# Optimization experiments

Hardware: AMD Instinct MI355X
Metric: run time of the kernel (lower is better)

Reference implementation:

```python
import jax, jax.numpy as jnp
import numpy as np

B, T, C = 2, 2048, 2048
N_HEAD, N_KV = 16, 4
HD = C // N_HEAD          # 128
ROPE_THETA = 10000.0


def setup_inputs() -> dict:
    key = jax.random.key(0)
    ks = jax.random.split(key, 6)
    std = 0.02
    x = jax.random.normal(ks[0], (B, T, C), dtype=jnp.float32)
    Wq = jax.random.normal(ks[1], (C, C), dtype=jnp.float32) * std
    Wk = jax.random.normal(ks[2], (C, N_KV * HD), dtype=jnp.float32) * std
    Wv = jax.random.normal(ks[3], (C, N_KV * HD), dtype=jnp.float32) * std
    Wo = jax.random.normal(ks[4], (C, C), dtype=jnp.float32) * std
    # real RoPE frequencies: freqs_cis = exp(i * t * theta^{-2j/hd})
    inv_freq = 1.0 / (ROPE_THETA ** (jnp.arange(0, HD, 2, dtype=jnp.float32) / HD))
    ang = jnp.arange(T, dtype=jnp.float32)[:, None] * inv_freq[None, :]  # [T, HD//2]
    return {"x": x, "Wq": Wq, "Wk": Wk, "Wv": Wv, "Wo": Wo,
            "freqs_cos": jnp.cos(ang), "freqs_sin": jnp.sin(ang)}


def _rope(t, cos, sin):
    # t: [B, H, T, HD]; cos/sin: [T, HD//2] -> complex rotate even/odd pairs
    tr = t.reshape(*t.shape[:-1], HD // 2, 2)
    re, im = tr[..., 0], tr[..., 1]
    c = cos[None, None, :, :]
    s = sin[None, None, :, :]
    out = jnp.stack([re * c - im * s, re * s + im * c], axis=-1)
    return out.reshape(t.shape)


def reference(x, Wq, Wk, Wv, Wo, freqs_cos, freqs_sin):
    Bm, Tm, Cm = x.shape
    q = (x @ Wq).reshape(Bm, Tm, N_HEAD, HD).transpose(0, 2, 1, 3)  # [B,H,T,HD]
    k = (x @ Wk).reshape(Bm, Tm, N_KV, HD).transpose(0, 2, 1, 3)    # [B,Hkv,T,HD]
    v = (x @ Wv).reshape(Bm, Tm, N_KV, HD).transpose(0, 2, 1, 3)
    q = _rope(q, freqs_cos, freqs_sin)
    k = _rope(k, freqs_cos, freqs_sin)
    rep = N_HEAD // N_KV
    k = jnp.repeat(k, rep, axis=1)  # GQA repeat_kv -> [B,H,T,HD]
    v = jnp.repeat(v, rep, axis=1)
    scale = 1.0 / jnp.sqrt(jnp.asarray(HD, dtype=x.dtype))
    att = jnp.einsum("bhqd,bhkd->bhqk", q, k) * scale
    causal = jnp.tril(jnp.ones((Tm, Tm), dtype=bool))
    att = jnp.where(causal[None, None], att, jnp.asarray(-jnp.inf, att.dtype))
    att = jax.nn.softmax(att, axis=-1)
    y = jnp.einsum("bhqk,bhkd->bhqd", att, v)
    y = y.transpose(0, 2, 1, 3).reshape(Bm, Tm, Cm)
    return y @ Wo
```

## Files before the change

### kernel.cpp

```cpp
#include <hip/hip_runtime.h>

#define B_ 2
#define T_ 2048
#define C_ 2048
#define NH_ 16
#define NKV_ 4
#define HD_ 128
#define REP_ (NH_ / NKV_)
#define LDQKV 3072

typedef unsigned short u16;
typedef __bf16 bf16x8v __attribute__((ext_vector_type(8)));
typedef float f32x4v __attribute__((ext_vector_type(4)));

__device__ __forceinline__ u16 f2bf(float f) {
    unsigned int u;
    __builtin_memcpy(&u, &f, 4);
    u += 0x7FFFu + ((u >> 16) & 1u);
    return (u16)(u >> 16);
}
__device__ __forceinline__ unsigned int pk2(float a, float b) {
    unsigned int ua, ub;
    __builtin_memcpy(&ua, &a, 4);
    __builtin_memcpy(&ub, &b, 4);
    ua += 0x8000u; ub += 0x8000u;
    return (ua >> 16) | (ub & 0xFFFF0000u);
}
__device__ __forceinline__ bf16x8v load8(const u16* p) {
    return *reinterpret_cast<const bf16x8v*>(p);
}
__device__ __forceinline__ void gl16(const u16* g, u16* l) {
    __builtin_amdgcn_global_load_lds(
        (const __attribute__((address_space(1))) void*)(g),
        (__attribute__((address_space(3))) void*)(l), 16, 0, 0);
}

__global__ void cvt_f32_bf16(const float* __restrict__ in, u16* __restrict__ out, int n4) {
    int i = blockIdx.x * blockDim.x + threadIdx.x;
    if (i >= n4) return;
    float4 v = reinterpret_cast<const float4*>(in)[i];
    ushort4 o;
    o.x = f2bf(v.x); o.y = f2bf(v.y); o.z = f2bf(v.z); o.w = f2bf(v.w);
    reinterpret_cast<ushort4*>(out)[i] = o;
}

__global__ void xpose_f32_bf16(const float* __restrict__ in, u16* __restrict__ out,
                               int R, int Cc) {
    __shared__ u16 tile[32][33];
    int bx = blockIdx.x * 32, by = blockIdx.y * 32;
    int tx = threadIdx.x, ty = threadIdx.y;
    for (int i = 0; i < 32; i += 8)
        tile[ty + i][tx] = f2bf(in[(size_t)(by + ty + i) * Cc + bx + tx]);
    __syncthreads();
    for (int i = 0; i < 32; i += 8)
        out[(size_t)(bx + ty + i) * R + by + tx] = tile[tx][ty + i];
}

__global__ __launch_bounds__(256) void gemm_qkv(const u16* __restrict__ A,
                                                const u16* __restrict__ BT,
                                                u16* __restrict__ Cq,
                                                u16* __restrict__ vtb,
                                                const float* __restrict__ cb,
                                                const float* __restrict__ sb,
                                                int M, int N, int K) {
    __shared__ __align__(16) u16 As[128 * 64];
    __shared__ __align__(16) u16 Bs[128 * 64];
    int tid = threadIdx.x;
    int lane = tid & 63, wave = tid >> 6;
    int wm = wave & 1, wn = wave >> 1;
    int m15 = lane & 15, quad = lane >> 4;
    int m0 = blockIdx.y * 128, n0 = blockIdx.x * 128;

    int r_ = tid >> 3, c_ = tid & 7;
    int gch = c_ ^ (r_ & 7);
    const u16* gA = A + (size_t)(m0 + r_) * K + gch * 8;
    const u16* gB = BT + (size_t)(n0 + r_) * K + gch * 8;
    u16* lA = As + tid * 8;
    u16* lB = Bs + tid * 8;

    int sw8 = m15 & 7;
    const u16* a0 = As + (wm * 64 + m15) * 64;
    const u16* b0 = Bs + (wn * 64 + m15) * 64;

    f32x4v acc[4][4] = {};
    for (int k0 = 0; k0 < K; k0 += 64) {
        __syncthreads();
        for (int j = 0; j < 4; j++) {
            gl16(gA + (size_t)(32 * j) * K, lA + j * 2048);
            gl16(gB + (size_t)(32 * j) * K, lB + j * 2048);
        }
        gA += 64; gB += 64;
        __syncthreads();
        for (int kc = 0; kc < 2; kc++) {
            int co = ((kc * 4 + quad) ^ sw8) * 8;
            bf16x8v af[4], bfv[4];
            for (int t = 0; t < 4; t++) {
                af[t] = load8(a0 + t * 1024 + co);
                bfv[t] = load8(b0 + t * 1024 + co);
            }
            for (int mt = 0; mt < 4; mt++)
                for (int nt = 0; nt < 4; nt++)
                    acc[mt][nt] = __builtin_amdgcn_mfma_f32_16x16x32_bf16(
                        af[mt], bfv[nt], acc[mt][nt], 0, 0, 0);
        }
    }

    if (n0 >= 2560) {
        for (int mt = 0; mt < 4; mt++)
            for (int nt = 0; nt < 4; nt++) {
                int hd = n0 + wn * 64 + nt * 16 + m15 - 2560;
                int mbase = m0 + wm * 64 + mt * 16 + quad * 4;
                int bb = mbase >> 11, tok = mbase & 2047;
                int g = (tok & 31) >> 2;
                int off = (tok & ~31) + ((g & 3) * 8 + (g >> 2) * 4);
                ushort4 pk;
                pk.x = f2bf(acc[mt][nt][0]);
                pk.y = f2bf(acc[mt][nt][1]);
                pk.z = f2bf(acc[mt][nt][2]);
                pk.w = f2bf(acc[mt][nt][3]);
                *reinterpret_cast<ushort4*>(vtb + ((size_t)bb * 512 + hd) * T_ + off) = pk;
            }
    } else {
        for (int mt = 0; mt < 4; mt++)
            for (int nt = 0; nt < 4; nt++) {
                int c = n0 + wn * 64 + nt * 16 + m15;
                int i = (c & 127) >> 1;
                float sgn = (c & 1) ? 1.f : -1.f;
                for (int r = 0; r < 4; r++) {
                    int mrow = m0 + wm * 64 + mt * 16 + quad * 4 + r;
                    int tok = mrow & 2047;
                    float cv = cb[tok * 64 + i];
                    float sv = sb[tok * 64 + i];
                    float v = acc[mt][nt][r];
                    float pval = __shfl_xor(v, 1, 64);
                    float outv = fmaf(v, cv, pval * sv * sgn);
                    Cq[(size_t)mrow * N + c] = f2bf(outv);
                }
            }
    }
}

__global__ __launch_bounds__(256) void gemm_out(const u16* __restrict__ A,
                                                const u16* __restrict__ BT,
                                                float* __restrict__ C,
                                                int M, int N, int K) {
    __shared__ __align__(16) u16 As[128 * 64];
    __shared__ __align__(16) u16 Bs[128 * 64];
    int tid = threadIdx.x;
    int lane = tid & 63, wave = tid >> 6;
    int wm = wave & 1, wn = wave >> 1;
    int m15 = lane & 15, quad = lane >> 4;
    int m0 = blockIdx.y * 128, n0 = blockIdx.x * 128;

    int r_ = tid >> 3, c_ = tid & 7;
    int gch = c_ ^ (r_ & 7);
    const u16* gA = A + (size_t)(m0 + r_) * K + gch * 8;
    const u16* gB = BT + (size_t)(n0 + r_) * K + gch * 8;
    u16* lA = As + tid * 8;
    u16* lB = Bs + tid * 8;

    int sw8 = m15 & 7;
    const u16* a0 = As + (wm * 64 + m15) * 64;
    const u16* b0 = Bs + (wn * 64 + m15) * 64;

    f32x4v acc[4][4] = {};
    for (int k0 = 0; k0 < K; k0 += 64) {
        __syncthreads();
        for (int j = 0; j < 4; j++) {
            gl16(gA + (size_t)(32 * j) * K, lA + j * 2048);
            gl16(gB + (size_t)(32 * j) * K, lB + j * 2048);
        }
        gA += 64; gB += 64;
        __syncthreads();
        for (int kc = 0; kc < 2; kc++) {
            int co = ((kc * 4 + quad) ^ sw8) * 8;
            bf16x8v af[4], bfv[4];
            for (int t = 0; t < 4; t++) {
                af[t] = load8(a0 + t * 1024 + co);
                bfv[t] = load8(b0 + t * 1024 + co);
            }
            for (int mt = 0; mt < 4; mt++)
                for (int nt = 0; nt < 4; nt++)
                    acc[mt][nt] = __builtin_amdgcn_mfma_f32_16x16x32_bf16(
                        af[mt], bfv[nt], acc[mt][nt], 0, 0, 0);
        }
    }

    for (int mt = 0; mt < 4; mt++)
        for (int nt = 0; nt < 4; nt++) {
            int c = n0 + wn * 64 + nt * 16 + m15;
            for (int r = 0; r < 4; r++) {
                int mrow = m0 + wm * 64 + mt * 16 + quad * 4 + r;
                C[(size_t)mrow * N + c] = acc[mt][nt][r];
            }
        }
}

__device__ __forceinline__ void stage_k128(const u16* kB, u16* Kl, int kt, int tid) {
    int keyc = tid >> 4, ch = tid & 15;
    const u16* g = kB + (size_t)(kt + keyc) * LDQKV + (ch ^ keyc) * 8;
    u16* l = Kl + tid * 8;
    for (int j = 0; j < 8; j++) {
        gl16(g, l);
        g += (size_t)16 * LDQKV;
        l += 2048;
    }
}
__device__ __forceinline__ void stage_v128(const u16* vB, u16* Vl, int kt, int tid) {
    int hdc = tid >> 4, ch = tid & 15;
    const u16* g = vB + (size_t)hdc * T_ + kt + (ch ^ hdc) * 8;
    u16* l = Vl + tid * 8;
    for (int j = 0; j < 8; j++) {
        gl16(g, l);
        g += (size_t)16 * T_;
        l += 2048;
    }
}

__global__ __launch_bounds__(256) void flash_k(const u16* __restrict__ qkv,
                                               const u16* __restrict__ vtb,
                                               u16* __restrict__ yb) {
    __shared__ __align__(16) u16 Kl[128 * 128];
    __shared__ __align__(16) u16 Vl[128 * 128];
    int h = blockIdx.y, b = blockIdx.z;
    int kv = h / REP_;
    int tid = threadIdx.x;
    int lane = tid & 63, wave = tid >> 6;
    int m15 = lane & 15, quad = lane >> 4;
    const u16* kB = qkv + (size_t)b * T_ * LDQKV + 2048 + kv * HD_;
    const u16* vB = vtb + ((size_t)(b * NKV_ + kv)) * HD_ * T_;
    const float scale2 = 0.1275173723f;
    const float M0b = 8.0f;
    const float NEG = -3.0e38f;

    for (int p = 0; p < 2; p++) {
        int qt = (p == 0) ? (int)blockIdx.x : (31 - (int)blockIdx.x);
        int qt0 = qt * 64;
        int qrow = qt0 + wave * 16;
        int q_i = qrow + m15;
        const u16* qp = qkv + (size_t)(b * T_ + q_i) * LDQKV + h * HD_ + quad * 8;
        bf16x8v qf[4];
        for (int kc = 0; kc < 4; kc++) qf[kc] = load8(qp + kc * 32);
        f32x4v o[8] = {};
        f32x4v lacc = {};

        int iters = qt0 / 128 + 1;
        for (int it = 0; it < iters; it++) {
            int kt = it * 128;
            __syncthreads();
            stage_k128(kB, Kl, kt, tid);
            stage_v128(vB, Vl, kt, tid);
            __syncthreads();
            f32x4v s4[8];
            for (int nt = 0; nt < 8; nt++) s4[nt] = (f32x4v){0.f, 0.f, 0.f, 0.f};
            for (int nt = 0; nt < 8; nt++) {
                const u16* kls = Kl + (nt * 16 + m15) * 128;
                for (int kc = 0; kc < 4; kc++)
                    s4[nt] = __builtin_amdgcn_mfma_f32_16x16x32_bf16(
                        load8(kls + (((kc * 4 + quad) ^ m15) * 8)), qf[kc], s4[nt], 0, 0, 0);
            }
            if (kt + 128 > qt0) {
                for (int nt = 0; nt < 8; nt++) {
                    int key = kt + nt * 16 + quad * 4;
                    for (int r = 0; r < 4; r++)
                        if (key + r > q_i) s4[nt][r] = NEG;
                }
            }
            for (int nt = 0; nt < 8; nt++) {
                for (int r = 0; r < 4; r++)
                    s4[nt][r] = exp2f(fmaf(s4[nt][r], scale2, -M0b));
                lacc += s4[nt];
            }
            for (int c = 0; c < 4; c++) {
                unsigned int w[4];
                w[0] = pk2(s4[2 * c][0], s4[2 * c][1]);
                w[1] = pk2(s4[2 * c][2], s4[2 * c][3]);
                w[2] = pk2(s4[2 * c + 1][0], s4[2 * c + 1][1]);
                w[3] = pk2(s4[2 * c + 1][2], s4[2 * c + 1][3]);
                bf16x8v pf;
                __builtin_memcpy(&pf, w, 16);
                for (int dt = 0; dt < 8; dt++) {
                    const u16* vls = Vl + (dt * 16 + m15) * 128;
                    o[dt] = __builtin_amdgcn_mfma_f32_16x16x32_bf16(
                        load8(vls + (((c * 4 + quad) ^ m15) * 8)), pf, o[dt], 0, 0, 0);
                }
            }
        }
        float l = lacc[0] + lacc[1] + lacc[2] + lacc[3];
        l += __shfl_xor(l, 16, 64);
        l += __shfl_xor(l, 32, 64);
        float inv = 1.f / l;
        u16* yp = yb + (size_t)(b * T_ + q_i) * C_ + h * HD_ + quad * 4;
        for (int dt = 0; dt < 8; dt++) {
            ushort4 pk;
            pk.x = f2bf(o[dt][0] * inv);
            pk.y = f2bf(o[dt][1] * inv);
            pk.z = f2bf(o[dt][2] * inv);
            pk.w = f2bf(o[dt][3] * inv);
            *reinterpret_cast<ushort4*>(yp + dt * 16) = pk;
        }
    }
}

extern "C" void kernel_launch(void* const* d_in, const int* in_sizes, int n_in,
                              void* d_out, int out_size, void* d_ws, size_t ws_size,
                              hipStream_t stream) {
    const float* x  = (const float*)d_in[0];
    const float* Wq = (const float*)d_in[1];
    const float* Wk = (const float*)d_in[2];
    const float* Wv = (const float*)d_in[3];
    const float* Wo = (const float*)d_in[4];
    const float* fc = (const float*)d_in[5];
    const float* fs = (const float*)d_in[6];
    float* out = (float*)d_out;

    char* ws = (char*)d_ws;
    u16* WqkvT = (u16*)(ws);
    u16* WoT   = (u16*)(ws + 12582912);
    u16* xb    = (u16*)(ws + 20971520);
    u16* qkvb  = (u16*)(ws + 37748736);
    u16* vtb   = (u16*)(ws + 62914560);
    u16* yb    = (u16*)(ws + 67108864);

    const int M = B_ * T_;

    int n4 = (M * C_) / 4;
    cvt_f32_bf16<<<n4 / 256, 256, 0, stream>>>(x, xb, n4);

    dim3 tb(32, 8);
    xpose_f32_bf16<<<dim3(C_ / 32, C_ / 32), tb, 0, stream>>>(Wq, WqkvT, C_, C_);
    xpose_f32_bf16<<<dim3((NKV_ * HD_) / 32, C_ / 32), tb, 0, stream>>>(Wk, WqkvT + 2048 * 2048, C_, NKV_ * HD_);
    xpose_f32_bf16<<<dim3((NKV_ * HD_) / 32, C_ / 32), tb, 0, stream>>>(Wv, WqkvT + 2560 * 2048, C_, NKV_ * HD_);
    xpose_f32_bf16<<<dim3(C_ / 32, C_ / 32), tb, 0, stream>>>(Wo, WoT, C_, C_);

    gemm_qkv<<<dim3(LDQKV / 128, M / 128), 256, 0, stream>>>(xb, WqkvT, qkvb, vtb, fc, fs, M, LDQKV, C_);

    flash_k<<<dim3(T_ / 128, NH_, B_), 256, 0, stream>>>(qkvb, vtb, yb);

    gemm_out<<<dim3(C_ / 128, M / 128), 256, 0, stream>>>(yb, WoT, out, M, C_, C_);
}
```

Measured before the change: 310.1 us.

## Use 256x256 double-buffered GEMM tiles with swizzled block order

Both projection GEMMs move from 128x128 tiles with 4 waves to 256x256 tiles with 8 waves. Each wave now computes a 128x64 sub-tile. Loads use a two-stage LDS double buffer with explicit vmcnt waits, so global fetches overlap MFMA work. A 1D grid with an XCD-aware block swizzle improves L2 locality, and setprio raises MFMA priority. In exchange, LDS use rises to 128KB per block and register pressure grows. Grid counts shrink: 192 blocks for QKV and 128 for the output GEMM, which may underfill the 256 CUs.

```diff
diff --git a/kernel.cpp b/kernel.cpp
--- a/kernel.cpp
+++ b/kernel.cpp
@@ -56,60 +56,94 @@
         out[(size_t)(bx + ty + i) * R + by + tx] = tile[tx][ty + i];
 }
 
-__global__ __launch_bounds__(256) void gemm_qkv(const u16* __restrict__ A,
-                                                const u16* __restrict__ BT,
-                                                u16* __restrict__ Cq,
-                                                u16* __restrict__ vtb,
-                                                const float* __restrict__ cb,
-                                                const float* __restrict__ sb,
-                                                int M, int N, int K) {
-    __shared__ __align__(16) u16 As[128 * 64];
-    __shared__ __align__(16) u16 Bs[128 * 64];
+__device__ __forceinline__ void stage_ab(const u16* gA, const u16* gB,
+                                         u16* As, u16* Bs, int tid, int K) {
+    u16* lA = As + tid * 8;
+    u16* lB = Bs + tid * 8;
+#pragma unroll
+    for (int j = 0; j < 4; j++) gl16(gA + (size_t)(64 * j) * K, lA + j * 4096);
+#pragma unroll
+    for (int j = 0; j < 4; j++) gl16(gB + (size_t)(64 * j) * K, lB + j * 4096);
+}
+
+__global__ __launch_bounds__(512, 2) void gemm_qkv(const u16* __restrict__ A,
+                                                   const u16* __restrict__ BT,
+                                                   u16* __restrict__ Cq,
+                                                   u16* __restrict__ vtb,
+                                                   const float* __restrict__ cb,
+                                                   const float* __restrict__ sb,
+                                                   int M, int N, int K) {
+    __shared__ __align__(16) u16 As[2][256 * 64];
+    __shared__ __align__(16) u16 Bs[2][256 * 64];
     int tid = threadIdx.x;
     int lane = tid & 63, wave = tid >> 6;
-    int wm = wave & 1, wn = wave >> 1;
+    int wm = wave >> 2, wn = wave & 3;
     int m15 = lane & 15, quad = lane >> 4;
-    int m0 = blockIdx.y * 128, n0 = blockIdx.x * 128;
+
+    int nbx = N >> 8;
+    int nwg = gridDim.x;
+    int bid = blockIdx.x;
+    int cpx = nwg >> 3;
+    int swz = (bid & 7) * cpx + (bid >> 3);
+    int bx = swz % nbx, by = swz / nbx;
+    int m0 = by * 256, n0 = bx * 256;
 
     int r_ = tid >> 3, c_ = tid & 7;
-    int gch = c_ ^ (r_ & 7);
-    const u16* gA = A + (size_t)(m0 + r_) * K + gch * 8;
-    const u16* gB = BT + (size_t)(n0 + r_) * K + gch * 8;
-    u16* lA = As + tid * 8;
-    u16* lB = Bs + tid * 8;
+    const u16* gA = A + (size_t)(m0 + r_) * K + (c_ ^ (r_ & 7)) * 8;
+    const u16* gB = BT + (size_t)(n0 + r_) * K + (c_ ^ (r_ & 7)) * 8;
 
     int sw8 = m15 & 7;
-    const u16* a0 = As + (wm * 64 + m15) * 64;
-    const u16* b0 = Bs + (wn * 64 + m15) * 64;
-
-    f32x4v acc[4][4] = {};
-    for (int k0 = 0; k0 < K; k0 += 64) {
-        __syncthreads();
-        for (int j = 0; j < 4; j++) {
-            gl16(gA + (size_t)(32 * j) * K, lA + j * 2048);
-            gl16(gB + (size_t)(32 * j) * K, lB + j * 2048);
-        }
-        gA += 64; gB += 64;
-        __syncthreads();
+    const u16* a0b = &As[0][0] + (wm * 128 + m15) * 64;
+    const u16* b0b = &Bs[0][0] + (wn * 64 + m15) * 64;
+
+    f32x4v acc[8][4] = {};
+
+    stage_ab(gA, gB, As[0], Bs[0], tid, K);
+    __builtin_amdgcn_sched_barrier(0);
+    stage_ab(gA + 64, gB + 64, As[1], Bs[1], tid, K);
+    asm volatile("s_waitcnt vmcnt(8)" ::: "memory");
+    __builtin_amdgcn_sched_barrier(0);
+    __builtin_amdgcn_s_barrier();
+
+    int NT = K >> 6;
+    for (int t = 0; t < NT; t++) {
+        const u16* a0 = a0b + (t & 1) * (256 * 64);
+        const u16* b0 = b0b + (t & 1) * (256 * 64);
+#pragma unroll
         for (int kc = 0; kc < 2; kc++) {
             int co = ((kc * 4 + quad) ^ sw8) * 8;
-            bf16x8v af[4], bfv[4];
-            for (int t = 0; t < 4; t++) {
-                af[t] = load8(a0 + t * 1024 + co);
-                bfv[t] = load8(b0 + t * 1024 + co);
-            }
-            for (int mt = 0; mt < 4; mt++)
+            bf16x8v bfv[4], af[8];
+#pragma unroll
+            for (int nt = 0; nt < 4; nt++) bfv[nt] = load8(b0 + nt * 1024 + co);
+#pragma unroll
+            for (int mt = 0; mt < 8; mt++) af[mt] = load8(a0 + mt * 1024 + co);
+            __builtin_amdgcn_s_setprio(1);
+#pragma unroll
+            for (int mt = 0; mt < 8; mt++)
+#pragma unroll
                 for (int nt = 0; nt < 4; nt++)
                     acc[mt][nt] = __builtin_amdgcn_mfma_f32_16x16x32_bf16(
                         af[mt], bfv[nt], acc[mt][nt], 0, 0, 0);
-        }
+            __builtin_amdgcn_s_setprio(0);
+        }
+        __builtin_amdgcn_s_barrier();
+        if (t + 2 < NT) {
+            stage_ab(gA + (t + 2) * 64, gB + (t + 2) * 64, As[t & 1], Bs[t & 1], tid, K);
+            asm volatile("s_waitcnt vmcnt(8)" ::: "memory");
+        } else {
+            asm volatile("s_waitcnt vmcnt(0)" ::: "memory");
+        }
+        __builtin_amdgcn_sched_barrier(0);
+        __builtin_amdgcn_s_barrier();
     }
 
     if (n0 >= 2560) {
-        for (int mt = 0; mt < 4; mt++)
+#pragma unroll
+        for (int mt = 0; mt < 8; mt++)
+#pragma unroll
             for (int nt = 0; nt < 4; nt++) {
                 int hd = n0 + wn * 64 + nt * 16 + m15 - 2560;
-                int mbase = m0 + wm * 64 + mt * 16 + quad * 4;
+                int mbase = m0 + wm * 128 + mt * 16 + quad * 4;
                 int bb = mbase >> 11, tok = mbase & 2047;
                 int g = (tok & 31) >> 2;
                 int off = (tok & ~31) + ((g & 3) * 8 + (g >> 2) * 4);
@@ -121,13 +155,16 @@
                 *reinterpret_cast<ushort4*>(vtb + ((size_t)bb * 512 + hd) * T_ + off) = pk;
             }
     } else {
-        for (int mt = 0; mt < 4; mt++)
+#pragma unroll
+        for (int mt = 0; mt < 8; mt++)
+#pragma unroll
             for (int nt = 0; nt < 4; nt++) {
                 int c = n0 + wn * 64 + nt * 16 + m15;
                 int i = (c & 127) >> 1;
                 float sgn = (c & 1) ? 1.f : -1.f;
+#pragma unroll
                 for (int r = 0; r < 4; r++) {
-                    int mrow = m0 + wm * 64 + mt * 16 + quad * 4 + r;
+                    int mrow = m0 + wm * 128 + mt * 16 + quad * 4 + r;
                     int tok = mrow & 2047;
                     float cv = cb[tok * 64 + i];
                     float sv = sb[tok * 64 + i];
@@ -140,57 +177,82 @@
     }
 }
 
-__global__ __launch_bounds__(256) void gemm_out(const u16* __restrict__ A,
-                                                const u16* __restrict__ BT,
-                                                float* __restrict__ C,
-                                                int M, int N, int K) {
-    __shared__ __align__(16) u16 As[128 * 64];
-    __shared__ __align__(16) u16 Bs[128 * 64];
+__global__ __launch_bounds__(512, 2) void gemm_out(const u16* __restrict__ A,
+                                                   const u16* __restrict__ BT,
+                                                   float* __restrict__ C,
+                                                   int M, int N, int K) {
+    __shared__ __align__(16) u16 As[2][256 * 64];
+    __shared__ __align__(16) u16 Bs[2][256 * 64];
     int tid = threadIdx.x;
     int lane = tid & 63, wave = tid >> 6;
-    int wm = wave & 1, wn = wave >> 1;
+    int wm = wave >> 2, wn = wave & 3;
     int m15 = lane & 15, quad = lane >> 4;
-    int m0 = blockIdx.y * 128, n0 = blockIdx.x * 128;
+
+    int nbx = N >> 8;
+    int nwg = gridDim.x;
+    int bid = blockIdx.x;
+    int cpx = nwg >> 3;
+    int swz = (bid & 7) * cpx + (bid >> 3);
+    int bx = swz % nbx, by = swz / nbx;
+    int m0 = by * 256, n0 = bx * 256;
 
     int r_ = tid >> 3, c_ = tid & 7;
-    int gch = c_ ^ (r_ & 7);
-    const u16* gA = A + (size_t)(m0 + r_) * K + gch * 8;
-    const u16* gB = BT + (size_t)(n0 + r_) * K + gch * 8;
-    u16* lA = As + tid * 8;
-    u16* lB = Bs + tid * 8;
+    const u16* gA = A + (size_t)(m0 + r_) * K + (c_ ^ (r_ & 7)) * 8;
+    const u16* gB = BT + (size_t)(n0 + r_) * K + (c_ ^ (r_ & 7)) * 8;
 
     int sw8 = m15 & 7;
-    const u16* a0 = As + (wm * 64 + m15) * 64;
-    const u16* b0 = Bs + (wn * 64 + m15) * 64;
-
-    f32x4v acc[4][4] = {};
-    for (int k0 = 0; k0 < K; k0 += 64) {
-        __syncthreads();
-        for (int j = 0; j < 4; j++) {
-            gl16(gA + (size_t)(32 * j) * K, lA + j * 2048);
-            gl16(gB + (size_t)(32 * j) * K, lB + j * 2048);
-        }
-        gA += 64; gB += 64;
-        __syncthreads();
+    const u16* a0b = &As[0][0] + (wm * 128 + m15) * 64;
+    const u16* b0b = &Bs[0][0] + (wn * 64 + m15) * 64;
+
+    f32x4v acc[8][4] = {};
+
+    stage_ab(gA, gB, As[0], Bs[0], tid, K);
+    __builtin_amdgcn_sched_barrier(0);
+    stage_ab(gA + 64, gB + 64, As[1], Bs[1], tid, K);
+    asm volatile("s_waitcnt vmcnt(8)" ::: "memory");
+    __builtin_amdgcn_sched_barrier(0);
+    __builtin_amdgcn_s_barrier();
+
+    int NT = K >> 6;
+    for (int t = 0; t < NT; t++) {
+        const u16* a0 = a0b + (t & 1) * (256 * 64);
+        const u16* b0 = b0b + (t & 1) * (256 * 64);
+#pragma unroll
         for (int kc = 0; kc < 2; kc++) {
             int co = ((kc * 4 + quad) ^ sw8) * 8;
-            bf16x8v af[4], bfv[4];
-            for (int t = 0; t < 4; t++) {
-                af[t] = load8(a0 + t * 1024 + co);
-                bfv[t] = load8(b0 + t * 1024 + co);
-            }
-            for (int mt = 0; mt < 4; mt++)
+            bf16x8v bfv[4], af[8];
+#pragma unroll
+            for (int nt = 0; nt < 4; nt++) bfv[nt] = load8(b0 + nt * 1024 + co);
+#pragma unroll
+            for (int mt = 0; mt < 8; mt++) af[mt] = load8(a0 + mt * 1024 + co);
+            __builtin_amdgcn_s_setprio(1);
+#pragma unroll
+            for (int mt = 0; mt < 8; mt++)
+#pragma unroll
                 for (int nt = 0; nt < 4; nt++)
                     acc[mt][nt] = __builtin_amdgcn_mfma_f32_16x16x32_bf16(
                         af[mt], bfv[nt], acc[mt][nt], 0, 0, 0);
-        }
-    }
-
-    for (int mt = 0; mt < 4; mt++)
+            __builtin_amdgcn_s_setprio(0);
+        }
+        __builtin_amdgcn_s_barrier();
+        if (t + 2 < NT) {
+            stage_ab(gA + (t + 2) * 64, gB + (t + 2) * 64, As[t & 1], Bs[t & 1], tid, K);
+            asm volatile("s_waitcnt vmcnt(8)" ::: "memory");
+        } else {
+            asm volatile("s_waitcnt vmcnt(0)" ::: "memory");
+        }
+        __builtin_amdgcn_sched_barrier(0);
+        __builtin_amdgcn_s_barrier();
+    }
+
+#pragma unroll
+    for (int mt = 0; mt < 8; mt++)
+#pragma unroll
         for (int nt = 0; nt < 4; nt++) {
             int c = n0 + wn * 64 + nt * 16 + m15;
+#pragma unroll
             for (int r = 0; r < 4; r++) {
-                int mrow = m0 + wm * 64 + mt * 16 + quad * 4 + r;
+                int mrow = m0 + wm * 128 + mt * 16 + quad * 4 + r;
                 C[(size_t)mrow * N + c] = acc[mt][nt][r];
             }
         }
@@ -333,9 +395,9 @@
     xpose_f32_bf16<<<dim3((NKV_ * HD_) / 32, C_ / 32), tb, 0, stream>>>(Wv, WqkvT + 2560 * 2048, C_, NKV_ * HD_);
     xpose_f32_bf16<<<dim3(C_ / 32, C_ / 32), tb, 0, stream>>>(Wo, WoT, C_, C_);
 
-    gemm_qkv<<<dim3(LDQKV / 128, M / 128), 256, 0, stream>>>(xb, WqkvT, qkvb, vtb, fc, fs, M, LDQKV, C_);
+    gemm_qkv<<<dim3((LDQKV / 256) * (M / 256)), 512, 0, stream>>>(xb, WqkvT, qkvb, vtb, fc, fs, M, LDQKV, C_);
 
     flash_k<<<dim3(T_ / 128, NH_, B_), 256, 0, stream>>>(qkvb, vtb, yb);
 
-    gemm_out<<<dim3(C_ / 128, M / 128), 256, 0, stream>>>(yb, WoT, out, M, C_, C_);
-}
+    gemm_out<<<dim3((C_ / 256) * (M / 256)), 512, 0, stream>>>(yb, WoT, out, M, C_, C_);
+}
```

Measured after the change: 321.9 us. +3.8%, slower.
